# Kernel tuning notes

Hardware: AMD Instinct MI355X
Metric: run time of the kernel (lower is better)

## Reference

```python
import jax, jax.numpy as jnp
import numpy as np

B, N, IN_DIM, HEADS, OUT_DIM = 8, 2048, 256, 4, 64
NEG_SLOPE = 0.2


def setup_inputs() -> dict:
    key = jax.random.key(0)
    k_h, k_w, k_as, k_ad = jax.random.split(key, 4)
    h = jax.random.normal(k_h, (B, N, IN_DIM), dtype=jnp.float32)
    # xavier-uniform-like scales
    w_lim = float(np.sqrt(6.0 / (IN_DIM + HEADS * OUT_DIM)))
    a_lim = float(np.sqrt(6.0 / (HEADS + OUT_DIM)))
    W = jax.random.uniform(k_w, (IN_DIM, HEADS * OUT_DIM), jnp.float32, -w_lim, w_lim)
    a_src = jax.random.uniform(k_as, (HEADS, OUT_DIM), jnp.float32, -a_lim, a_lim)
    a_dst = jax.random.uniform(k_ad, (HEADS, OUT_DIM), jnp.float32, -a_lim, a_lim)
    bias = jnp.zeros((HEADS * OUT_DIM,), jnp.float32)
    mask = jnp.ones((B, N), dtype=bool)
    return {"h": h, "W": W, "a_src": a_src, "a_dst": a_dst, "bias": bias, "mask": mask}


def reference(h, W, a_src, a_dst, bias, mask):
    Bn, Nn, _ = h.shape
    Hh, Dd = a_src.shape
    # Wh: [B, H, N, D]
    Wh = (h @ W).reshape(Bn, Nn, Hh, Dd).transpose(0, 2, 1, 3)
    el = jnp.einsum("bhnd,hd->bhn", Wh, a_src)  # [B,H,N]
    er = jnp.einsum("bhnd,hd->bhn", Wh, a_dst)  # [B,H,N]
    # e[b,h,i,j] = leaky_relu(el[b,h,i] + er[b,h,j])
    e = jax.nn.leaky_relu(el[..., :, None] + er[..., None, :], NEG_SLOPE)
    e = jnp.where(mask[:, None, None, :], e, jnp.float32(-1e9))
    alpha = jax.nn.softmax(e, axis=-1)  # over source nodes j (dropout=0/eval)
    h_prime = jnp.einsum("bhij,bhjd->bhid", alpha, Wh)  # [B,H,N,D]
    h_prime = h_prime.transpose(0, 2, 1, 3).reshape(Bn, Nn, Hh * Dd)  # concat heads
    return h_prime + bias
```

## Files before the change

### kernel.cpp

```cpp
#include <hip/hip_runtime.h>
#include <math.h>

#define B_   8
#define N_   2048
#define IN_  256
#define H_   4
#define D_   64
#define C_   256
#define M_   (B_*N_)
#define NEG  0.2f
#define LOG2E 1.4426950408889634f

typedef short bf16x8 __attribute__((ext_vector_type(8)));
typedef float f32x4  __attribute__((ext_vector_type(4)));

__device__ inline uint cvt_pk_bf16(float lo, float hi) {
    uint r;
    asm("v_cvt_pk_bf16_f32 %0, %1, %2" : "=v"(r) : "v"(lo), "v"(hi));
    return r;
}

__device__ inline void split8(const float v[8], bf16x8* hi, bf16x8* lo) {
    union { bf16x8 v; uint u[4]; } H, L;
    #pragma unroll
    for (int j = 0; j < 4; j++) {
        float a = v[2 * j], b = v[2 * j + 1];
        uint ph = cvt_pk_bf16(a, b);
        float ra = a - __uint_as_float(ph << 16);
        float rb = b - __uint_as_float(ph & 0xFFFF0000u);
        H.u[j] = ph;
        L.u[j] = cvt_pk_bf16(ra, rb);
    }
    *hi = H.v; *lo = L.v;
}

__global__ __launch_bounds__(256) void wprep_kernel(const float* __restrict__ W,
                                                    ushort* __restrict__ Wt_hi,
                                                    ushort* __restrict__ Wt_lo) {
    const int t = threadIdx.x, blk = blockIdx.x;
    float v[4];
    #pragma unroll
    for (int kk = 0; kk < 4; kk++) v[kk] = W[(blk * 4 + kk) * 256 + t];
    uint h0 = cvt_pk_bf16(v[0], v[1]);
    uint h1 = cvt_pk_bf16(v[2], v[3]);
    uint l0 = cvt_pk_bf16(v[0] - __uint_as_float(h0 << 16),
                          v[1] - __uint_as_float(h0 & 0xFFFF0000u));
    uint l1 = cvt_pk_bf16(v[2] - __uint_as_float(h1 << 16),
                          v[3] - __uint_as_float(h1 & 0xFFFF0000u));
    *(uint2*)&Wt_hi[(size_t)t * 256 + blk * 4] = make_uint2(h0, h1);
    *(uint2*)&Wt_lo[(size_t)t * 256 + blk * 4] = make_uint2(l0, l1);
}

#define BP 264
#define EP 136

__global__ __launch_bounds__(256, 2) void gemm_fused(const float* __restrict__ h,
                                                     const ushort* __restrict__ Wt_hi,
                                                     const ushort* __restrict__ Wt_lo,
                                                     const float* __restrict__ a_src,
                                                     const float* __restrict__ a_dst,
                                                     ushort* __restrict__ Wht,
                                                     float* __restrict__ Ee,
                                                     float* __restrict__ Ff,
                                                     float* __restrict__ Gg) {
    __shared__ ushort Bs_h[64 * BP], Bs_l[64 * BP];

    const int t = threadIdx.x;
    const int m0 = blockIdx.x * 128;
    const int nb = blockIdx.y;
    const int b  = m0 >> 11;
    const int wid = t >> 6, lane = t & 63;
    const int c16 = lane & 15, quad = lane >> 4;

    {
        const int c = t >> 2, kq = t & 3;
        const ushort* sh = Wt_hi + (size_t)(nb * 64 + c) * 256 + kq * 64;
        const ushort* sl = Wt_lo + (size_t)(nb * 64 + c) * 256 + kq * 64;
        ushort* dh = &Bs_h[c * BP + kq * 64];
        ushort* dl = &Bs_l[c * BP + kq * 64];
        #pragma unroll
        for (int q = 0; q < 8; q++) {
            *(uint4*)(dh + q * 8) = *(const uint4*)(sh + q * 8);
            *(uint4*)(dl + q * 8) = *(const uint4*)(sl + q * 8);
        }
    }

    const int row0 = m0 + wid * 32 + c16;
    const float* hp0 = h + (size_t)row0 * 256 + quad * 8;
    const float* hp1 = hp0 + 16 * 256;

    float4 p0a = *(const float4*)hp0, p0b = *(const float4*)(hp0 + 4);
    float4 p1a = *(const float4*)hp1, p1b = *(const float4*)(hp1 + 4);

    __syncthreads();

    f32x4 acc[2][4] = {};
    for (int k0 = 0; k0 < 256; k0 += 32) {
        float v0[8] = {p0a.x, p0a.y, p0a.z, p0a.w, p0b.x, p0b.y, p0b.z, p0b.w};
        float v1[8] = {p1a.x, p1a.y, p1a.z, p1a.w, p1b.x, p1b.y, p1b.z, p1b.w};
        if (k0 < 224) {
            p0a = *(const float4*)(hp0 + k0 + 32); p0b = *(const float4*)(hp0 + k0 + 36);
            p1a = *(const float4*)(hp1 + k0 + 32); p1b = *(const float4*)(hp1 + k0 + 36);
        }
        bf16x8 ah0, al0, ah1, al1;
        split8(v0, &ah0, &al0);
        split8(v1, &ah1, &al1);
        #pragma unroll
        for (int fc = 0; fc < 4; fc++) {
            bf16x8 bhf = *(const bf16x8*)&Bs_h[(fc * 16 + c16) * BP + k0 + quad * 8];
            bf16x8 blf = *(const bf16x8*)&Bs_l[(fc * 16 + c16) * BP + k0 + quad * 8];
            acc[0][fc] = __builtin_amdgcn_mfma_f32_16x16x32_bf16(ah0, bhf, acc[0][fc], 0, 0, 0);
            acc[0][fc] = __builtin_amdgcn_mfma_f32_16x16x32_bf16(al0, bhf, acc[0][fc], 0, 0, 0);
            acc[0][fc] = __builtin_amdgcn_mfma_f32_16x16x32_bf16(ah0, blf, acc[0][fc], 0, 0, 0);
            acc[1][fc] = __builtin_amdgcn_mfma_f32_16x16x32_bf16(ah1, bhf, acc[1][fc], 0, 0, 0);
            acc[1][fc] = __builtin_amdgcn_mfma_f32_16x16x32_bf16(al1, bhf, acc[1][fc], 0, 0, 0);
            acc[1][fc] = __builtin_amdgcn_mfma_f32_16x16x32_bf16(ah1, blf, acc[1][fc], 0, 0, 0);
        }
    }

    {
        float avs[4], avd[4];
        #pragma unroll
        for (int fc = 0; fc < 4; fc++) {
            avs[fc] = a_src[nb * 64 + fc * 16 + c16];
            avd[fc] = a_dst[nb * 64 + fc * 16 + c16];
        }
        float ds[2][4] = {}, dd[2][4] = {};
        #pragma unroll
        for (int rw = 0; rw < 2; rw++)
            #pragma unroll
            for (int r = 0; r < 4; r++)
                #pragma unroll
                for (int fc = 0; fc < 4; fc++) {
                    ds[rw][r] += acc[rw][fc][r] * avs[fc];
                    dd[rw][r] += acc[rw][fc][r] * avd[fc];
                }
        #pragma unroll
        for (int off = 1; off < 16; off <<= 1)
            #pragma unroll
            for (int rw = 0; rw < 2; rw++)
                #pragma unroll
                for (int r = 0; r < 4; r++) {
                    ds[rw][r] += __shfl_xor(ds[rw][r], off);
                    dd[rw][r] += __shfl_xor(dd[rw][r], off);
                }
        if (c16 == 0) {
            #pragma unroll
            for (int rw = 0; rw < 2; rw++)
                #pragma unroll
                for (int r = 0; r < 4; r++) {
                    int m = m0 + wid * 32 + rw * 16 + quad * 4 + r;
                    int idx = (b * 4 + nb) * N_ + (m & 2047);
                    float ee = ds[rw][r] * LOG2E;
                    float rr = dd[rw][r] * LOG2E;
                    Ee[idx] = __builtin_amdgcn_exp2f(rr);
                    Ff[idx] = __builtin_amdgcn_exp2f(NEG * rr);
                    Gg[idx] = __builtin_amdgcn_exp2f(-0.8f * ee);
                }
        }
    }

    __syncthreads();
    ushort* Es = Bs_h;
    #pragma unroll
    for (int rw = 0; rw < 2; rw++) {
        const int nloc = wid * 32 + rw * 16 + quad * 4;
        #pragma unroll
        for (int fc = 0; fc < 4; fc++) {
            const int d = fc * 16 + c16;
            uint2 pk = make_uint2(cvt_pk_bf16(acc[rw][fc][0], acc[rw][fc][1]),
                                  cvt_pk_bf16(acc[rw][fc][2], acc[rw][fc][3]));
            *(uint2*)&Es[d * EP + nloc] = pk;
        }
    }
    __syncthreads();
    {
        const int d = t >> 2, ch = t & 3;
        ushort* dst = Wht + ((size_t)(b * 4 + nb) * 64 + d) * N_ + (m0 & 2047) + ch * 32;
        const ushort* srcl = &Es[d * EP + ch * 32];
        #pragma unroll
        for (int q = 0; q < 4; q++)
            *(uint4*)(dst + q * 8) = *(const uint4*)(srcl + q * 8);
    }
}

#define TP2 144

__global__ __launch_bounds__(256, 2) void attn_kernel(const ushort* __restrict__ Wht,
                                                      const float* __restrict__ Ee,
                                                      const float* __restrict__ Ff,
                                                      const float* __restrict__ Gg,
                                                      const float* __restrict__ bias,
                                                      float* __restrict__ out) {
    __shared__ ushort Whs[2][64 * TP2];
    __shared__ float E_s[2][128], F_s[2][128];
    const int t = threadIdx.x;
    const int bh = blockIdx.x, b = bh >> 2, hh = bh & 3;
    const int wid = t >> 6, lane = t & 63;
    const int c16 = lane & 15, quad = lane >> 4;
    const int ibase = blockIdx.y * 128 + wid * 32;
    const int sd = t >> 3, sch = t & 7;

    float Gi[2];
    #pragma unroll
    for (int g = 0; g < 2; g++) Gi[g] = Gg[bh * N_ + ibase + g * 16 + c16];

    f32x4 acc[2][4] = {};
    f32x4 den[2] = {};
    const bf16x8 ones = {0x3F80, 0x3F80, 0x3F80, 0x3F80,
                         0x3F80, 0x3F80, 0x3F80, 0x3F80};
    const ushort* WhtB = Wht + (size_t)bh * 64 * N_;
    const float* Eb = Ee + (size_t)bh * N_;
    const float* Fb = Ff + (size_t)bh * N_;

    uint4 w00 = *(const uint4*)(WhtB + (size_t)sd * N_ + sch * 8);
    uint4 w01 = *(const uint4*)(WhtB + (size_t)sd * N_ + 64 + sch * 8);
    uint4 w10 = *(const uint4*)(WhtB + (size_t)(sd + 32) * N_ + sch * 8);
    uint4 w11 = *(const uint4*)(WhtB + (size_t)(sd + 32) * N_ + 64 + sch * 8);
    float ev_e = 0.f, ev_f = 0.f;
    if (t < 128) { ev_e = Eb[t]; ev_f = Fb[t]; }

    for (int jt = 0; jt < 16; jt++) {
        const int buf = jt & 1;
        *(uint4*)&Whs[buf][sd * TP2 + sch * 8]             = w00;
        *(uint4*)&Whs[buf][sd * TP2 + 64 + sch * 8]        = w01;
        *(uint4*)&Whs[buf][(sd + 32) * TP2 + sch * 8]      = w10;
        *(uint4*)&Whs[buf][(sd + 32) * TP2 + 64 + sch * 8] = w11;
        if (t < 128) { E_s[buf][t] = ev_e; F_s[buf][t] = ev_f; }
        if (jt < 15) {
            const int j1 = (jt + 1) * 128;
            w00 = *(const uint4*)(WhtB + (size_t)sd * N_ + j1 + sch * 8);
            w01 = *(const uint4*)(WhtB + (size_t)sd * N_ + j1 + 64 + sch * 8);
            w10 = *(const uint4*)(WhtB + (size_t)(sd + 32) * N_ + j1 + sch * 8);
            w11 = *(const uint4*)(WhtB + (size_t)(sd + 32) * N_ + j1 + 64 + sch * 8);
            if (t < 128) { ev_e = Eb[j1 + t]; ev_f = Fb[j1 + t]; }
        }
        __syncthreads();
        #pragma unroll
        for (int ks = 0; ks < 4; ks++) {
            const int jb = ks * 32 + quad * 8;
            float4 e0 = *(const float4*)&E_s[buf][jb];
            float4 e1 = *(const float4*)&E_s[buf][jb + 4];
            float4 f0 = *(const float4*)&F_s[buf][jb];
            float4 f1 = *(const float4*)&F_s[buf][jb + 4];
            float E8[8] = {e0.x, e0.y, e0.z, e0.w, e1.x, e1.y, e1.z, e1.w};
            float F8[8] = {f0.x, f0.y, f0.z, f0.w, f1.x, f1.y, f1.z, f1.w};
            bf16x8 bfr[4];
            #pragma unroll
            for (int fd = 0; fd < 4; fd++)
                bfr[fd] = *(const bf16x8*)&Whs[buf][(fd * 16 + c16) * TP2 + jb];
            #pragma unroll
            for (int g = 0; g < 2; g++) {
                const float gi = Gi[g];
                union { bf16x8 v; uint u[4]; } af;
                #pragma unroll
                for (int j = 0; j < 4; j++) {
                    float qa = fmaxf(E8[2 * j],     gi * F8[2 * j]);
                    float qb = fmaxf(E8[2 * j + 1], gi * F8[2 * j + 1]);
                    af.u[j] = cvt_pk_bf16(qa, qb);
                }
                #pragma unroll
                for (int fd = 0; fd < 4; fd++)
                    acc[g][fd] = __builtin_amdgcn_mfma_f32_16x16x32_bf16(af.v, bfr[fd], acc[g][fd], 0, 0, 0);
                den[g] = __builtin_amdgcn_mfma_f32_16x16x32_bf16(af.v, ones, den[g], 0, 0, 0);
            }
        }
    }

    float bl[4];
    #pragma unroll
    for (int fd = 0; fd < 4; fd++) bl[fd] = bias[hh * 64 + fd * 16 + c16];
    #pragma unroll
    for (int g = 0; g < 2; g++)
        #pragma unroll
        for (int r = 0; r < 4; r++) {
            int i = ibase + g * 16 + quad * 4 + r;
            float inv = 1.0f / den[g][r];
            float* dst = out + (size_t)(b * N_ + i) * C_ + hh * 64;
            #pragma unroll
            for (int fd = 0; fd < 4; fd++)
                dst[fd * 16 + c16] = acc[g][fd][r] * inv + bl[fd];
        }
}

extern "C" void kernel_launch(void* const* d_in, const int* in_sizes, int n_in,
                              void* d_out, int out_size, void* d_ws, size_t ws_size,
                              hipStream_t stream) {
    const float* h     = (const float*)d_in[0];
    const float* W     = (const float*)d_in[1];
    const float* a_src = (const float*)d_in[2];
    const float* a_dst = (const float*)d_in[3];
    const float* bias  = (const float*)d_in[4];
    float* out = (float*)d_out;

    ushort* Wt_hi = (ushort*)d_ws;
    ushort* Wt_lo = Wt_hi + 256 * 256;
    ushort* Wht   = Wt_lo + 256 * 256;
    float*  Ee    = (float*)(Wht + (size_t)M_ * C_);
    float*  Ff    = Ee + 32 * N_;
    float*  Gg    = Ff + 32 * N_;

    wprep_kernel<<<64, 256, 0, stream>>>(W, Wt_hi, Wt_lo);
    gemm_fused<<<dim3(M_ / 128, 4), 256, 0, stream>>>(h, Wt_hi, Wt_lo, a_src, a_dst,
                                                      Wht, Ee, Ff, Gg);
    attn_kernel<<<dim3(32, 16), 256, 0, stream>>>(Wht, Ee, Ff, Gg, bias, out);
}
```

Before: 119.1 us.

## Fold attention vectors into W and drop low-part of W split

Precomputes W·a_src and W·a_dst per head in the weight-prep kernel, so the attention logits come from a direct fp32 dot product of h with these folded vectors instead of reducing the GEMM accumulators. The W low-bf16 residual is removed, cutting the MFMA count from three to two per tile and freeing its shared memory. Tiles shrink to 64 rows with a higher occupancy bound. Projected features lose some precision because W is only represented in bf16-hi, but the logits stay in fp32.

```diff
diff --git a/kernel.cpp b/kernel.cpp
--- a/kernel.cpp
+++ b/kernel.cpp
@@ -35,38 +35,54 @@
 }
 
 __global__ __launch_bounds__(256) void wprep_kernel(const float* __restrict__ W,
+                                                    const float* __restrict__ a_src,
+                                                    const float* __restrict__ a_dst,
                                                     ushort* __restrict__ Wt_hi,
-                                                    ushort* __restrict__ Wt_lo) {
+                                                    float* __restrict__ Ub) {
     const int t = threadIdx.x, blk = blockIdx.x;
+    const int wid = t >> 6, lane = t & 63;
     float v[4];
     #pragma unroll
     for (int kk = 0; kk < 4; kk++) v[kk] = W[(blk * 4 + kk) * 256 + t];
     uint h0 = cvt_pk_bf16(v[0], v[1]);
     uint h1 = cvt_pk_bf16(v[2], v[3]);
-    uint l0 = cvt_pk_bf16(v[0] - __uint_as_float(h0 << 16),
-                          v[1] - __uint_as_float(h0 & 0xFFFF0000u));
-    uint l1 = cvt_pk_bf16(v[2] - __uint_as_float(h1 << 16),
-                          v[3] - __uint_as_float(h1 & 0xFFFF0000u));
     *(uint2*)&Wt_hi[(size_t)t * 256 + blk * 4] = make_uint2(h0, h1);
-    *(uint2*)&Wt_lo[(size_t)t * 256 + blk * 4] = make_uint2(l0, l1);
+
+    const float as = a_src[t], ad = a_dst[t];
+    float ps[4], pd[4];
+    #pragma unroll
+    for (int kk = 0; kk < 4; kk++) { ps[kk] = v[kk] * as; pd[kk] = v[kk] * ad; }
+    #pragma unroll
+    for (int off = 1; off < 64; off <<= 1)
+        #pragma unroll
+        for (int kk = 0; kk < 4; kk++) {
+            ps[kk] += __shfl_xor(ps[kk], off);
+            pd[kk] += __shfl_xor(pd[kk], off);
+        }
+    if (lane == 0) {
+        #pragma unroll
+        for (int kk = 0; kk < 4; kk++) {
+            Ub[wid * 512 + blk * 4 + kk]       = ps[kk];
+            Ub[wid * 512 + 256 + blk * 4 + kk] = pd[kk];
+        }
+    }
 }
 
 #define BP 264
-#define EP 136
-
-__global__ __launch_bounds__(256, 2) void gemm_fused(const float* __restrict__ h,
+#define EP 74
+
+__global__ __launch_bounds__(256, 4) void gemm_fused(const float* __restrict__ h,
                                                      const ushort* __restrict__ Wt_hi,
-                                                     const ushort* __restrict__ Wt_lo,
-                                                     const float* __restrict__ a_src,
-                                                     const float* __restrict__ a_dst,
+                                                     const float* __restrict__ Ub,
                                                      ushort* __restrict__ Wht,
                                                      float* __restrict__ Ee,
                                                      float* __restrict__ Ff,
                                                      float* __restrict__ Gg) {
-    __shared__ ushort Bs_h[64 * BP], Bs_l[64 * BP];
+    __shared__ ushort Bs_h[64 * BP];
+    __shared__ float us[256], ud[256];
 
     const int t = threadIdx.x;
-    const int m0 = blockIdx.x * 128;
+    const int m0 = blockIdx.x * 64;
     const int nb = blockIdx.y;
     const int b  = m0 >> 11;
     const int wid = t >> 6, lane = t & 63;
@@ -75,112 +91,84 @@
     {
         const int c = t >> 2, kq = t & 3;
         const ushort* sh = Wt_hi + (size_t)(nb * 64 + c) * 256 + kq * 64;
-        const ushort* sl = Wt_lo + (size_t)(nb * 64 + c) * 256 + kq * 64;
         ushort* dh = &Bs_h[c * BP + kq * 64];
-        ushort* dl = &Bs_l[c * BP + kq * 64];
-        #pragma unroll
-        for (int q = 0; q < 8; q++) {
+        #pragma unroll
+        for (int q = 0; q < 8; q++)
             *(uint4*)(dh + q * 8) = *(const uint4*)(sh + q * 8);
-            *(uint4*)(dl + q * 8) = *(const uint4*)(sl + q * 8);
-        }
-    }
-
-    const int row0 = m0 + wid * 32 + c16;
+    }
+    us[t] = Ub[nb * 512 + t];
+    ud[t] = Ub[nb * 512 + 256 + t];
+
+    const int row0 = m0 + wid * 16 + c16;
     const float* hp0 = h + (size_t)row0 * 256 + quad * 8;
-    const float* hp1 = hp0 + 16 * 256;
 
     float4 p0a = *(const float4*)hp0, p0b = *(const float4*)(hp0 + 4);
-    float4 p1a = *(const float4*)hp1, p1b = *(const float4*)(hp1 + 4);
 
     __syncthreads();
 
-    f32x4 acc[2][4] = {};
+    f32x4 acc[4] = {};
+    float ds = 0.f, dd = 0.f;
     for (int k0 = 0; k0 < 256; k0 += 32) {
         float v0[8] = {p0a.x, p0a.y, p0a.z, p0a.w, p0b.x, p0b.y, p0b.z, p0b.w};
-        float v1[8] = {p1a.x, p1a.y, p1a.z, p1a.w, p1b.x, p1b.y, p1b.z, p1b.w};
         if (k0 < 224) {
             p0a = *(const float4*)(hp0 + k0 + 32); p0b = *(const float4*)(hp0 + k0 + 36);
-            p1a = *(const float4*)(hp1 + k0 + 32); p1b = *(const float4*)(hp1 + k0 + 36);
-        }
-        bf16x8 ah0, al0, ah1, al1;
-        split8(v0, &ah0, &al0);
-        split8(v1, &ah1, &al1);
+        }
+        {
+            float4 u0 = *(const float4*)&us[k0 + quad * 8];
+            float4 u1 = *(const float4*)&us[k0 + quad * 8 + 4];
+            float4 w0 = *(const float4*)&ud[k0 + quad * 8];
+            float4 w1 = *(const float4*)&ud[k0 + quad * 8 + 4];
+            ds += v0[0]*u0.x + v0[1]*u0.y + v0[2]*u0.z + v0[3]*u0.w
+                + v0[4]*u1.x + v0[5]*u1.y + v0[6]*u1.z + v0[7]*u1.w;
+            dd += v0[0]*w0.x + v0[1]*w0.y + v0[2]*w0.z + v0[3]*w0.w
+                + v0[4]*w1.x + v0[5]*w1.y + v0[6]*w1.z + v0[7]*w1.w;
+        }
+        bf16x8 ah, al;
+        split8(v0, &ah, &al);
         #pragma unroll
         for (int fc = 0; fc < 4; fc++) {
             bf16x8 bhf = *(const bf16x8*)&Bs_h[(fc * 16 + c16) * BP + k0 + quad * 8];
-            bf16x8 blf = *(const bf16x8*)&Bs_l[(fc * 16 + c16) * BP + k0 + quad * 8];
-            acc[0][fc] = __builtin_amdgcn_mfma_f32_16x16x32_bf16(ah0, bhf, acc[0][fc], 0, 0, 0);
-            acc[0][fc] = __builtin_amdgcn_mfma_f32_16x16x32_bf16(al0, bhf, acc[0][fc], 0, 0, 0);
-            acc[0][fc] = __builtin_amdgcn_mfma_f32_16x16x32_bf16(ah0, blf, acc[0][fc], 0, 0, 0);
-            acc[1][fc] = __builtin_amdgcn_mfma_f32_16x16x32_bf16(ah1, bhf, acc[1][fc], 0, 0, 0);
-            acc[1][fc] = __builtin_amdgcn_mfma_f32_16x16x32_bf16(al1, bhf, acc[1][fc], 0, 0, 0);
-            acc[1][fc] = __builtin_amdgcn_mfma_f32_16x16x32_bf16(ah1, blf, acc[1][fc], 0, 0, 0);
-        }
-    }
-
-    {
-        float avs[4], avd[4];
-        #pragma unroll
-        for (int fc = 0; fc < 4; fc++) {
-            avs[fc] = a_src[nb * 64 + fc * 16 + c16];
-            avd[fc] = a_dst[nb * 64 + fc * 16 + c16];
-        }
-        float ds[2][4] = {}, dd[2][4] = {};
-        #pragma unroll
-        for (int rw = 0; rw < 2; rw++)
-            #pragma unroll
-            for (int r = 0; r < 4; r++)
-                #pragma unroll
-                for (int fc = 0; fc < 4; fc++) {
-                    ds[rw][r] += acc[rw][fc][r] * avs[fc];
-                    dd[rw][r] += acc[rw][fc][r] * avd[fc];
-                }
-        #pragma unroll
-        for (int off = 1; off < 16; off <<= 1)
-            #pragma unroll
-            for (int rw = 0; rw < 2; rw++)
-                #pragma unroll
-                for (int r = 0; r < 4; r++) {
-                    ds[rw][r] += __shfl_xor(ds[rw][r], off);
-                    dd[rw][r] += __shfl_xor(dd[rw][r], off);
-                }
-        if (c16 == 0) {
-            #pragma unroll
-            for (int rw = 0; rw < 2; rw++)
-                #pragma unroll
-                for (int r = 0; r < 4; r++) {
-                    int m = m0 + wid * 32 + rw * 16 + quad * 4 + r;
-                    int idx = (b * 4 + nb) * N_ + (m & 2047);
-                    float ee = ds[rw][r] * LOG2E;
-                    float rr = dd[rw][r] * LOG2E;
-                    Ee[idx] = __builtin_amdgcn_exp2f(rr);
-                    Ff[idx] = __builtin_amdgcn_exp2f(NEG * rr);
-                    Gg[idx] = __builtin_amdgcn_exp2f(-0.8f * ee);
-                }
+            acc[fc] = __builtin_amdgcn_mfma_f32_16x16x32_bf16(ah, bhf, acc[fc], 0, 0, 0);
+            acc[fc] = __builtin_amdgcn_mfma_f32_16x16x32_bf16(al, bhf, acc[fc], 0, 0, 0);
+        }
+    }
+
+    {
+        #pragma unroll
+        for (int off = 16; off < 64; off <<= 1) {
+            ds += __shfl_xor(ds, off);
+            dd += __shfl_xor(dd, off);
+        }
+        if (quad == 0) {
+            int m = m0 + wid * 16 + c16;
+            int idx = (b * 4 + nb) * N_ + (m & 2047);
+            float ee = ds * LOG2E;
+            float rr = dd * LOG2E;
+            Ee[idx] = __builtin_amdgcn_exp2f(rr);
+            Ff[idx] = __builtin_amdgcn_exp2f(NEG * rr);
+            Gg[idx] = __builtin_amdgcn_exp2f(-0.8f * ee);
         }
     }
 
     __syncthreads();
     ushort* Es = Bs_h;
-    #pragma unroll
-    for (int rw = 0; rw < 2; rw++) {
-        const int nloc = wid * 32 + rw * 16 + quad * 4;
+    {
+        const int nloc = wid * 16 + quad * 4;
         #pragma unroll
         for (int fc = 0; fc < 4; fc++) {
             const int d = fc * 16 + c16;
-            uint2 pk = make_uint2(cvt_pk_bf16(acc[rw][fc][0], acc[rw][fc][1]),
-                                  cvt_pk_bf16(acc[rw][fc][2], acc[rw][fc][3]));
+            uint2 pk = make_uint2(cvt_pk_bf16(acc[fc][0], acc[fc][1]),
+                                  cvt_pk_bf16(acc[fc][2], acc[fc][3]));
             *(uint2*)&Es[d * EP + nloc] = pk;
         }
     }
     __syncthreads();
     {
         const int d = t >> 2, ch = t & 3;
-        ushort* dst = Wht + ((size_t)(b * 4 + nb) * 64 + d) * N_ + (m0 & 2047) + ch * 32;
-        const ushort* srcl = &Es[d * EP + ch * 32];
-        #pragma unroll
-        for (int q = 0; q < 4; q++)
-            *(uint4*)(dst + q * 8) = *(const uint4*)(srcl + q * 8);
+        ushort* dst = Wht + ((size_t)(b * 4 + nb) * 64 + d) * N_ + (m0 & 2047) + ch * 16;
+        const ushort* srcl = &Es[d * EP + ch * 16];
+        *(uint4*)(dst)     = *(const uint4*)(srcl);
+        *(uint4*)(dst + 8) = *(const uint4*)(srcl + 8);
     }
 }
 
@@ -294,14 +282,13 @@
     float* out = (float*)d_out;
 
     ushort* Wt_hi = (ushort*)d_ws;
-    ushort* Wt_lo = Wt_hi + 256 * 256;
-    ushort* Wht   = Wt_lo + 256 * 256;
+    float*  Ub    = (float*)(Wt_hi + 256 * 256);
+    ushort* Wht   = (ushort*)(Ub + 4 * 512);
     float*  Ee    = (float*)(Wht + (size_t)M_ * C_);
     float*  Ff    = Ee + 32 * N_;
     float*  Gg    = Ff + 32 * N_;
 
-    wprep_kernel<<<64, 256, 0, stream>>>(W, Wt_hi, Wt_lo);
-    gemm_fused<<<dim3(M_ / 128, 4), 256, 0, stream>>>(h, Wt_hi, Wt_lo, a_src, a_dst,
-                                                      Wht, Ee, Ff, Gg);
+    wprep_kernel<<<64, 256, 0, stream>>>(W, a_src, a_dst, Wt_hi, Ub);
+    gemm_fused<<<dim3(M_ / 64, 4), 256, 0, stream>>>(h, Wt_hi, Ub, Wht, Ee, Ff, Gg);
     attn_kernel<<<dim3(32, 16), 256, 0, stream>>>(Wht, Ee, Ff, Gg, bias, out);
 }
```

Measured after the change: 116.3 us, median of 2. 2.4% less time.
